# Kernel optimization log

Measured on AMD Instinct MI355X. Metric: run time of the kernel, lower is better.

Reference implementation:

```python
import jax, jax.numpy as jnp
import numpy as np

HIDDEN_DIM = 8


def setup_inputs() -> dict:
    key = jax.random.key(0)
    ks = jax.random.split(key, 10)
    B, S, C, H = 2048, 200, 25, HIDDEN_DIM
    s = 0.1
    return {
        "x": jax.random.normal(ks[0], (B, S, C), jnp.float32),
        "delay_W": jax.random.normal(ks[1], (S, C), jnp.float32) * s,
        "delay_b": jax.random.normal(ks[2], (S,), jnp.float32) * s,
        "U_W": jax.random.normal(ks[3], (H, C), jnp.float32) * s,
        "U_b": jax.random.normal(ks[4], (H,), jnp.float32) * s,
        "A_W": jax.random.normal(ks[5], (H, H), jnp.float32) * s,
        "B_W": jax.random.normal(ks[6], (H, C), jnp.float32) * s,
        "B_b": jax.random.normal(ks[7], (H,), jnp.float32) * s,
        "out_W": jax.random.normal(ks[8], (C, H), jnp.float32) * s,
        "out_b": jax.random.normal(ks[9], (C,), jnp.float32) * s,
    }


def reference(x, delay_W, delay_b, U_W, U_b, A_W, B_W, B_b, out_W, out_b):
    # x: [B, S, C] -> [S, B, C]
    xt = jnp.swapaxes(x, 0, 1)
    S, B, C = xt.shape
    # synaptic delay: each source timestep t distributes its signal over
    # all output timesteps via a softmax over the TIMESTEPS axis.
    logits = xt @ delay_W.T + delay_b                # [S, B, S]
    w = jax.nn.softmax(logits, axis=-1)              # [S, B, S_out]
    x_del = jnp.einsum('tbc,tbs->sbc', xt, w)        # [S_out, B, C]
    # SSM inputs
    u = x_del @ U_W.T + U_b                          # [S, B, H]
    b = jax.nn.sigmoid(x_del @ B_W.T + B_b)          # [S, B, H]

    # linear recurrence h_t = h_{t-1} A^T + b_t * u_t, h_0 = 0
    def step(h, bu):
        b_t, u_t = bu
        h = h @ A_W.T + b_t * u_t
        return h, h

    h0 = jnp.zeros((B, HIDDEN_DIM), xt.dtype)
    _, hs = jax.lax.scan(step, h0, (b, u))           # [S, B, H]
    out = hs @ out_W.T + out_b                       # [S, B, C]
    return jnp.swapaxes(out, 0, 1)                   # [B, S, C]
```

## Files before the change

kernel.cpp:

```cpp
#include <hip/hip_runtime.h>

#define NB 2048
#define S_ 200
#define C_ 25
#define H_ 8
#define WROWS 208
#define STR 28
#define NSTRIP 13
#define NSTILE 13
#define NPAIR 7
#define XDS 28
#define WFRAG (13 * 64 * 4)

typedef __bf16   bf16x8 __attribute__((ext_vector_type(8)));
typedef float    f32x4  __attribute__((ext_vector_type(4)));
typedef unsigned uint4v __attribute__((ext_vector_type(4)));

struct Frag { bf16x8 hi, lo; };

__device__ __forceinline__ unsigned short f2bf(float f) {
    unsigned u = __builtin_bit_cast(unsigned, f);
    return (unsigned short)((u + 0x7FFFu + ((u >> 16) & 1u)) >> 16);
}
__device__ __forceinline__ float bfh2f(unsigned short h) {
    return __builtin_bit_cast(float, (unsigned)h << 16);
}
__device__ __forceinline__ unsigned hi_pair(unsigned d0, unsigned d1) {
    return (d0 & 0xFFFFu) | (d1 << 16);
}
__device__ __forceinline__ unsigned lo_pair(unsigned d0, unsigned d1) {
    return (d0 >> 16) | (d1 & 0xFFFF0000u);
}
__device__ __forceinline__ Frag build_frag8(uint4v d0, uint4v d1) {
    uint4v h, l;
    h.x = hi_pair(d0.x, d0.y); h.y = hi_pair(d0.z, d0.w);
    h.z = hi_pair(d1.x, d1.y); h.w = hi_pair(d1.z, d1.w);
    l.x = lo_pair(d0.x, d0.y); l.y = lo_pair(d0.z, d0.w);
    l.z = lo_pair(d1.x, d1.y); l.w = lo_pair(d1.z, d1.w);
    Frag f;
    f.hi = __builtin_bit_cast(bf16x8, h);
    f.lo = __builtin_bit_cast(bf16x8, l);
    return f;
}
__device__ __forceinline__ bf16x8 build_hi8(uint4v d0, uint4v d1) {
    uint4v h;
    h.x = hi_pair(d0.x, d0.y); h.y = hi_pair(d0.z, d0.w);
    h.z = hi_pair(d1.x, d1.y); h.w = hi_pair(d1.z, d1.w);
    return __builtin_bit_cast(bf16x8, h);
}
__device__ __forceinline__ f32x4 mfma16(bf16x8 a, bf16x8 b, f32x4 c) {
    return __builtin_amdgcn_mfma_f32_16x16x32_bf16(a, b, c, 0, 0, 0);
}
__device__ __forceinline__ f32x4 mfma_split(const Frag& a, const Frag& b, f32x4 c) {
    c = mfma16(a.hi, b.hi, c);
    c = mfma16(a.hi, b.lo, c);
    c = mfma16(a.lo, b.hi, c);
    return c;
}
__device__ __forceinline__ float fexp2(float x) {
    float r; asm("v_exp_f32 %0, %1" : "=v"(r) : "v"(x)); return r;
}
__device__ __forceinline__ float flog2(float x) {
    float r; asm("v_log_f32 %0, %1" : "=v"(r) : "v"(x)); return r;
}
__device__ __forceinline__ unsigned cvt_pk_bf16(float vlo, float vhi) {
    unsigned r; asm("v_cvt_pk_bf16_f32 %0, %1, %2" : "=v"(r) : "v"(vlo), "v"(vhi)); return r;
}
__device__ __forceinline__ float lo16f(unsigned p) { return __builtin_bit_cast(float, p << 16); }
__device__ __forceinline__ float hi16f(unsigned p) { return __builtin_bit_cast(float, p & 0xFFFF0000u); }
__device__ __forceinline__ void pack_hl2(float v0, float v1, unsigned& d0, unsigned& d1) {
    unsigned hp = cvt_pk_bf16(v0, v1);
    float r0 = v0 - lo16f(hp);
    float r1 = v1 - hi16f(hp);
    unsigned lp = cvt_pk_bf16(r0, r1);
    d0 = (hp & 0xFFFFu) | (lp << 16);
    d1 = (hp >> 16) | (lp & 0xFFFF0000u);
}

__device__ __forceinline__ void xpose_quads(unsigned& a0, unsigned& a1,
                                            unsigned& b0, unsigned& b1) {
    asm("v_permlane32_swap_b32 %0, %1" : "+v"(a0), "+v"(b0));
    asm("v_permlane32_swap_b32 %0, %1" : "+v"(a1), "+v"(b1));
    asm("v_permlane16_swap_b32 %0, %1" : "+v"(a0), "+v"(b0));
    asm("v_permlane16_swap_b32 %0, %1" : "+v"(a1), "+v"(b1));
}

template<bool GUARD>
__device__ __forceinline__ void build_b2h(const unsigned* X32p, int pair, int q, int n,
                                          bf16x8 b2h[2]) {
#pragma unroll
    for (int ct = 0; ct < 2; ++ct) {
        const int c = ct * 16 + n;
        uint4v d0, d1;
#pragma unroll
        for (int j = 0; j < 4; ++j) {
            int t2 = pair * 32 + q * 8 + j;
            unsigned v;
            if (GUARD) v = (t2 < WROWS) ? X32p[t2 * STR + c] : 0u;
            else       v = X32p[t2 * STR + c];
            ((unsigned*)&d0)[j] = v;
        }
#pragma unroll
        for (int j = 0; j < 4; ++j) {
            int t2 = pair * 32 + q * 8 + 4 + j;
            unsigned v;
            if (GUARD) v = (t2 < WROWS) ? X32p[t2 * STR + c] : 0u;
            else       v = X32p[t2 * STR + c];
            ((unsigned*)&d1)[j] = v;
        }
        b2h[ct] = build_hi8(d0, d1);
    }
}

__global__ void prep_w_kernel(const float* __restrict__ delay_W,
                              const float* __restrict__ A_W,
                              unsigned* __restrict__ ws) {
    const float LOG2E = 1.44269504088896340736f;
    unsigned* Whi = ws;
    unsigned* Wlo = ws + WFRAG;
    for (int idx = blockIdx.x * 256 + threadIdx.x; idx < WFRAG; idx += gridDim.x * 256) {
        int d = idx & 3, lane = (idx >> 2) & 63, sv = idx >> 8;
        int q = lane >> 4, nn = lane & 15;
        int s  = sv * 16 + nn;
        int c0 = q * 8 + 2 * d;
        float v0 = (s < S_ && c0     < C_) ? delay_W[s * C_ + c0]     * LOG2E : 0.f;
        float v1 = (s < S_ && c0 + 1 < C_) ? delay_W[s * C_ + c0 + 1] * LOG2E : 0.f;
        unsigned short h0 = f2bf(v0), h1 = f2bf(v1);
        unsigned short l0 = f2bf(v0 - bfh2f(h0)), l1 = f2bf(v1 - bfh2f(h1));
        Whi[idx] = (unsigned)h0 | ((unsigned)h1 << 16);
        Wlo[idx] = (unsigned)l0 | ((unsigned)l1 << 16);
    }
    __shared__ float A2s[64];
    __shared__ float A4s[64];
    if (blockIdx.x == 0) {
        float* A2g = (float*)(ws + 2 * WFRAG);
        float* A4g = (float*)(ws + 2 * WFRAG + 64);
        float* A8g = (float*)(ws + 2 * WFRAG + 128);
        const int i = threadIdx.x >> 3, j = threadIdx.x & 7;
        if (threadIdx.x < 64) {
            float s = 0.f;
            for (int k = 0; k < 8; ++k) s = fmaf(A_W[i * 8 + k], A_W[k * 8 + j], s);
            A2s[threadIdx.x] = s; A2g[threadIdx.x] = s;
        }
        __syncthreads();
        if (threadIdx.x < 64) {
            float s = 0.f;
            for (int k = 0; k < 8; ++k) s = fmaf(A2s[i * 8 + k], A2s[k * 8 + j], s);
            A4s[threadIdx.x] = s; A4g[threadIdx.x] = s;
        }
        __syncthreads();
        if (threadIdx.x < 64) {
            float s = 0.f;
            for (int k = 0; k < 8; ++k) s = fmaf(A4s[i * 8 + k], A4s[k * 8 + j], s);
            A8g[threadIdx.x] = s;
        }
    }
}

__global__ __launch_bounds__(256, 5) void ssm_syn_delay_kernel(
    const float* __restrict__ x,       const unsigned* __restrict__ ws,
    const float* __restrict__ delay_b, const float* __restrict__ U_W,
    const float* __restrict__ U_b,     const float* __restrict__ A_W,
    const float* __restrict__ B_W,     const float* __restrict__ B_b,
    const float* __restrict__ out_W,   const float* __restrict__ out_b,
    float* __restrict__ out)
{
    __shared__ __align__(16) unsigned X32[WROWS * STR + 4];
    __shared__ __align__(16) float lsed[WROWS];
    __shared__ __align__(16) float dbs_l[WROWS];

    const int tid  = threadIdx.x;
    const int wid  = tid >> 6;
    const int lane = tid & 63;
    const int q    = lane >> 4;
    const int n    = lane & 15;
    const int b    = blockIdx.x;
    const float* xb = x + (size_t)b * (S_ * C_);
    const unsigned* Whi = ws;
    const unsigned* Wlo = ws + WFRAG;
    const float* A2g = (const float*)(ws + 2 * WFRAG);
    const float* A4g = (const float*)(ws + 2 * WFRAG + 64);
    const float* A8g = (const float*)(ws + 2 * WFRAG + 128);

    for (int i = tid; i < WROWS * 7; i += 256) {
        int r = i / 7, cg = i - r * 7;
        f32x4 v = {0.f, 0.f, 0.f, 0.f};
        if (r < S_) {
            if (cg < 6)       __builtin_memcpy(&v, &xb[r * C_ + cg * 4], 16);
            else              v[0] = xb[r * C_ + 24];
        }
        unsigned e0, e1, e2, e3;
        pack_hl2(v[0], v[1], e0, e1);
        pack_hl2(v[2], v[3], e2, e3);
        uint4v p = {e0, e1, e2, e3};
        *(uint4v*)&X32[r * STR + cg * 4] = p;
    }
    if (tid == 0) {
        uint4v z = {0u, 0u, 0u, 0u};
        *(uint4v*)&X32[WROWS * STR] = z;
    }
    for (int i = tid; i < WROWS; i += 256)
        dbs_l[i] = (i < S_) ? delay_b[i] * 1.44269504088896340736f : -1e30f;
    __syncthreads();

    for (int st = wid; st < NSTRIP; st += 4) {
        const int t = st * 16 + n;
        const uint4v* xp = (const uint4v*)&X32[t * STR + q * 8];
        Frag fa = build_frag8(xp[0], xp[1]);
        float rs0 = 0.f, rs1 = 0.f, rs2 = 0.f, rs3 = 0.f;
        for (int sv = 0; sv < NSTILE; ++sv) {
            Frag fb;
            fb.hi = __builtin_bit_cast(bf16x8, *(const uint4v*)&Whi[(sv * 64 + lane) * 4]);
            fb.lo = __builtin_bit_cast(bf16x8, *(const uint4v*)&Wlo[(sv * 64 + lane) * 4]);
            f32x4 L = {0.f, 0.f, 0.f, 0.f};
            L = mfma_split(fa, fb, L);
            const float dbv = dbs_l[sv * 16 + n];
            rs0 += fexp2(L[0] + dbv);
            rs1 += fexp2(L[1] + dbv);
            rs2 += fexp2(L[2] + dbv);
            rs3 += fexp2(L[3] + dbv);
        }
#pragma unroll
        for (int off = 1; off < 16; off <<= 1) {
            rs0 += __shfl_xor(rs0, off);
            rs1 += __shfl_xor(rs1, off);
            rs2 += __shfl_xor(rs2, off);
            rs3 += __shfl_xor(rs3, off);
        }
        if (n < 4) {
            float v = (n == 0) ? rs0 : (n == 1) ? rs1 : (n == 2) ? rs2 : rs3;
            lsed[st * 16 + q * 4 + n] = flog2(v);
        }
    }
    __syncthreads();

    f32x4 acc[4][2];
#pragma unroll
    for (int i = 0; i < 4; ++i)
#pragma unroll
        for (int j = 0; j < 2; ++j) acc[i][j] = f32x4{0.f, 0.f, 0.f, 0.f};

    for (int pair = 0; pair < NPAIR; ++pair) {
        const int sA = 2 * pair, sB = sA + 1;
        const bool bval = (sB < NSTRIP);
        const uint4v* xpA = (const uint4v*)&X32[(sA * 16 + n) * STR + q * 8];
        Frag faA = build_frag8(xpA[0], xpA[1]);
        Frag faB;
        if (bval) {
            const uint4v* xpB = (const uint4v*)&X32[(sB * 16 + n) * STR + q * 8];
            faB = build_frag8(xpB[0], xpB[1]);
        }
        f32x4 lseA = *(const f32x4*)&lsed[sA * 16 + q * 4];
        f32x4 lseB = bval ? *(const f32x4*)&lsed[sB * 16 + q * 4] : f32x4{0,0,0,0};
        bf16x8 b2h[2];
        if (pair < 6) build_b2h<false>(X32, pair, q, n, b2h);
        else          build_b2h<true >(X32, pair, q, n, b2h);

#pragma unroll
        for (int si = 0; si < 4; ++si) {
            const int sv = wid + 4 * si;
            if (sv >= NSTILE) continue;
            Frag fb;
            fb.hi = __builtin_bit_cast(bf16x8, *(const uint4v*)&Whi[(sv * 64 + lane) * 4]);
            fb.lo = __builtin_bit_cast(bf16x8, *(const uint4v*)&Wlo[(sv * 64 + lane) * 4]);
            const float dbv = dbs_l[sv * 16 + n];
            unsigned pA0, pA1, qA0, qA1;
            {
                f32x4 L = {0.f, 0.f, 0.f, 0.f};
                L = mfma_split(faA, fb, L);
                float e0 = fexp2(L[0] + dbv - lseA[0]);
                float e1 = fexp2(L[1] + dbv - lseA[1]);
                float e2 = fexp2(L[2] + dbv - lseA[2]);
                float e3 = fexp2(L[3] + dbv - lseA[3]);
                pA0 = cvt_pk_bf16(e0, e1);
                pA1 = cvt_pk_bf16(e2, e3);
                qA0 = cvt_pk_bf16(e0 - lo16f(pA0), e1 - hi16f(pA0));
                qA1 = cvt_pk_bf16(e2 - lo16f(pA1), e3 - hi16f(pA1));
            }
            unsigned pB0 = 0u, pB1 = 0u, qB0 = 0u, qB1 = 0u;
            if (bval) {
                f32x4 L = {0.f, 0.f, 0.f, 0.f};
                L = mfma_split(faB, fb, L);
                float e0 = fexp2(L[0] + dbv - lseB[0]);
                float e1 = fexp2(L[1] + dbv - lseB[1]);
                float e2 = fexp2(L[2] + dbv - lseB[2]);
                float e3 = fexp2(L[3] + dbv - lseB[3]);
                pB0 = cvt_pk_bf16(e0, e1);
                pB1 = cvt_pk_bf16(e2, e3);
                qB0 = cvt_pk_bf16(e0 - lo16f(pB0), e1 - hi16f(pB0));
                qB1 = cvt_pk_bf16(e2 - lo16f(pB1), e3 - hi16f(pB1));
            }
            xpose_quads(pA0, pA1, pB0, pB1);
            xpose_quads(qA0, qA1, qB0, qB1);
            uint4v hv = {pA0, pA1, pB0, pB1};
            uint4v lv = {qA0, qA1, qB0, qB1};
            bf16x8 a2h = __builtin_bit_cast(bf16x8, hv);
            bf16x8 a2l = __builtin_bit_cast(bf16x8, lv);
#pragma unroll
            for (int ct = 0; ct < 2; ++ct) {
                f32x4 c4 = acc[si][ct];
                c4 = mfma16(a2h, b2h[ct], c4);
                c4 = mfma16(a2l, b2h[ct], c4);
                acc[si][ct] = c4;
            }
        }
    }
    __syncthreads();

    float* fbse = (float*)&X32[0];
    float* xdelf = fbse;
    float* pbuf  = fbse;
    float* r1    = fbse + 1600;
    float* r2    = fbse + 3200;
#pragma unroll
    for (int si = 0; si < 4; ++si) {
        const int sv = wid + 4 * si;
        if (sv >= NSTILE) continue;
#pragma unroll
        for (int ct = 0; ct < 2; ++ct) {
            const int c = ct * 16 + n;
            if (c < C_) {
#pragma unroll
                for (int r = 0; r < 4; ++r) {
                    const int s = sv * 16 + q * 4 + r;
                    if (s < S_) xdelf[s * XDS + c] = acc[si][ct][r];
                }
            }
        }
    }
    __syncthreads();

    {
        float a[24], a24 = 0.f;
        const bool act = tid < S_;
        if (act) {
            const f32x4* ar = (const f32x4*)&xdelf[tid * XDS];
#pragma unroll
            for (int k = 0; k < 6; ++k) *(f32x4*)&a[k * 4] = ar[k];
            a24 = xdelf[tid * XDS + 24];
        }
        __syncthreads();
        if (act) {
            const int s = tid;
#pragma unroll
            for (int h = 0; h < H_; ++h) {
                float uu = fmaf(a24, U_W[h * C_ + 24], U_b[h]);
                float bb = fmaf(a24, B_W[h * C_ + 24], B_b[h]);
#pragma unroll
                for (int i = 0; i < 24; ++i) {
                    uu = fmaf(a[i], U_W[h * C_ + i], uu);
                    bb = fmaf(a[i], B_W[h * C_ + i], bb);
                }
                float sg_ = 1.0f / (1.0f + __expf(-bb));
                pbuf[s * H_ + h] = uu * sg_;
            }
        }
    }
    __syncthreads();

    for (int i2 = tid; i2 < S_ * H_; i2 += 256) {
        const int s = i2 >> 3, i = i2 & 7;
        float v = pbuf[i2];
        if (s > 0) {
            const float* pm = &pbuf[(s - 1) * H_];
#pragma unroll
            for (int j = 0; j < H_; ++j) v = fmaf(A_W[i * H_ + j], pm[j], v);
        }
        r1[i2] = v;
    }
    __syncthreads();
    for (int i2 = tid; i2 < S_ * H_; i2 += 256) {
        const int s = i2 >> 3, i = i2 & 7;
        float v = r1[i2];
        if (s > 1) {
            const float* pm = &r1[(s - 2) * H_];
#pragma unroll
            for (int j = 0; j < H_; ++j) v = fmaf(A2g[i * H_ + j], pm[j], v);
        }
        r2[i2] = v;
    }
    __syncthreads();
    for (int i2 = tid; i2 < S_ * H_; i2 += 256) {
        const int s = i2 >> 3, i = i2 & 7;
        float v = r2[i2];
        if (s > 3) {
            const float* pm = &r2[(s - 4) * H_];
#pragma unroll
            for (int j = 0; j < H_; ++j) v = fmaf(A4g[i * H_ + j], pm[j], v);
        }
        pbuf[i2] = v;
    }
    __syncthreads();
    if (tid < 64) {
        const int r = tid >> 3, i = tid & 7;
        float A8r[H_];
#pragma unroll
        for (int j = 0; j < H_; ++j) A8r[j] = A8g[i * H_ + j];
        float h = 0.f;
        for (int k = 0; k < 25; ++k) {
            const int s = 8 * k + r;
            float v = pbuf[s * H_ + i];
#pragma unroll
            for (int j = 0; j < H_; ++j) v = fmaf(A8r[j], __shfl(h, j, 8), v);
            h = v;
            r1[s * H_ + i] = h;
        }
    }
    __syncthreads();

    float* ob_ptr = out + (size_t)b * (S_ * C_);
    for (int i = tid; i < S_ * C_; i += 256) {
        int s = i / C_, c = i - s * C_;
        const f32x4* pr = (const f32x4*)&r1[s * H_];
        const f32x4* wr = (const f32x4*)&out_W[c * H_];
        f32x4 h0 = pr[0], h1 = pr[1];
        f32x4 w0 = wr[0], w1 = wr[1];
        float v = out_b[c];
        v = fmaf(h0[0], w0[0], v);
        v = fmaf(h0[1], w0[1], v);
        v = fmaf(h0[2], w0[2], v);
        v = fmaf(h0[3], w0[3], v);
        v = fmaf(h1[0], w1[0], v);
        v = fmaf(h1[1], w1[1], v);
        v = fmaf(h1[2], w1[2], v);
        v = fmaf(h1[3], w1[3], v);
        ob_ptr[i] = v;
    }
}

extern "C" void kernel_launch(void* const* d_in, const int* in_sizes, int n_in,
                              void* d_out, int out_size, void* d_ws, size_t ws_size,
                              hipStream_t stream) {
    const float* x       = (const float*)d_in[0];
    const float* delay_W = (const float*)d_in[1];
    const float* delay_b = (const float*)d_in[2];
    const float* U_W     = (const float*)d_in[3];
    const float* U_b     = (const float*)d_in[4];
    const float* A_W     = (const float*)d_in[5];
    const float* B_W     = (const float*)d_in[6];
    const float* B_b     = (const float*)d_in[7];
    const float* out_W   = (const float*)d_in[8];
    const float* out_b   = (const float*)d_in[9];
    float* out = (float*)d_out;
    unsigned* ws = (unsigned*)d_ws;

    prep_w_kernel<<<4, 256, 0, stream>>>(delay_W, A_W, ws);
    ssm_syn_delay_kernel<<<NB, 256, 0, stream>>>(
        x, ws, delay_b, U_W, U_b, A_W, B_W, B_b, out_W, out_b, out);
}
```

Measured before the change: 231.1 us.

## Precompute transposed x B-fragments in LDS and batch logsumexp strips per W tile

Builds the transposed bf16 x fragments for the second GEMM once per block into a new shared-memory table, so each pair iteration reads one vector per tile instead of doing eight scalar strided loads and packing. The logsumexp pass now keeps up to four strip fragments in registers and loops over W tiles once, so each W fragment is loaded once per wave rather than once per strip. Occupancy hint drops from 5 to 4 waves per SIMD to make room for the added registers and about 14 KB of extra LDS.

```diff
diff --git a/kernel.cpp b/kernel.cpp
--- a/kernel.cpp
+++ b/kernel.cpp
@@ -11,6 +11,7 @@
 #define NPAIR 7
 #define XDS 28
 #define WFRAG (13 * 64 * 4)
+#define B2N (NPAIR * 2 * 64 * 4)
 
 typedef __bf16   bf16x8 __attribute__((ext_vector_type(8)));
 typedef float    f32x4  __attribute__((ext_vector_type(4)));
@@ -42,12 +43,6 @@
     f.lo = __builtin_bit_cast(bf16x8, l);
     return f;
 }
-__device__ __forceinline__ bf16x8 build_hi8(uint4v d0, uint4v d1) {
-    uint4v h;
-    h.x = hi_pair(d0.x, d0.y); h.y = hi_pair(d0.z, d0.w);
-    h.z = hi_pair(d1.x, d1.y); h.w = hi_pair(d1.z, d1.w);
-    return __builtin_bit_cast(bf16x8, h);
-}
 __device__ __forceinline__ f32x4 mfma16(bf16x8 a, bf16x8 b, f32x4 c) {
     return __builtin_amdgcn_mfma_f32_16x16x32_bf16(a, b, c, 0, 0, 0);
 }
@@ -83,33 +78,6 @@
     asm("v_permlane32_swap_b32 %0, %1" : "+v"(a1), "+v"(b1));
     asm("v_permlane16_swap_b32 %0, %1" : "+v"(a0), "+v"(b0));
     asm("v_permlane16_swap_b32 %0, %1" : "+v"(a1), "+v"(b1));
-}
-
-template<bool GUARD>
-__device__ __forceinline__ void build_b2h(const unsigned* X32p, int pair, int q, int n,
-                                          bf16x8 b2h[2]) {
-#pragma unroll
-    for (int ct = 0; ct < 2; ++ct) {
-        const int c = ct * 16 + n;
-        uint4v d0, d1;
-#pragma unroll
-        for (int j = 0; j < 4; ++j) {
-            int t2 = pair * 32 + q * 8 + j;
-            unsigned v;
-            if (GUARD) v = (t2 < WROWS) ? X32p[t2 * STR + c] : 0u;
-            else       v = X32p[t2 * STR + c];
-            ((unsigned*)&d0)[j] = v;
-        }
-#pragma unroll
-        for (int j = 0; j < 4; ++j) {
-            int t2 = pair * 32 + q * 8 + 4 + j;
-            unsigned v;
-            if (GUARD) v = (t2 < WROWS) ? X32p[t2 * STR + c] : 0u;
-            else       v = X32p[t2 * STR + c];
-            ((unsigned*)&d1)[j] = v;
-        }
-        b2h[ct] = build_hi8(d0, d1);
-    }
 }
 
 __global__ void prep_w_kernel(const float* __restrict__ delay_W,
@@ -157,7 +125,7 @@
     }
 }
 
-__global__ __launch_bounds__(256, 5) void ssm_syn_delay_kernel(
+__global__ __launch_bounds__(256, 4) void ssm_syn_delay_kernel(
     const float* __restrict__ x,       const unsigned* __restrict__ ws,
     const float* __restrict__ delay_b, const float* __restrict__ U_W,
     const float* __restrict__ U_b,     const float* __restrict__ A_W,
@@ -166,6 +134,7 @@
     float* __restrict__ out)
 {
     __shared__ __align__(16) unsigned X32[WROWS * STR + 4];
+    __shared__ __align__(16) unsigned B2T[B2N];
     __shared__ __align__(16) float lsed[WROWS];
     __shared__ __align__(16) float dbs_l[WROWS];
 
@@ -203,33 +172,62 @@
         dbs_l[i] = (i < S_) ? delay_b[i] * 1.44269504088896340736f : -1e30f;
     __syncthreads();
 
-    for (int st = wid; st < NSTRIP; st += 4) {
-        const int t = st * 16 + n;
-        const uint4v* xp = (const uint4v*)&X32[t * STR + q * 8];
-        Frag fa = build_frag8(xp[0], xp[1]);
-        float rs0 = 0.f, rs1 = 0.f, rs2 = 0.f, rs3 = 0.f;
+    for (int idx = tid; idx < B2N; idx += 256) {
+        const int k  = idx & 3;
+        const int ln = (idx >> 2) & 63;
+        const int ct = (idx >> 8) & 1;
+        const int pr = idx >> 9;
+        const int t0 = pr * 32 + (ln >> 4) * 8 + 2 * k;
+        const int c  = ct * 16 + (ln & 15);
+        unsigned u0 = (t0     < WROWS) ? X32[t0 * STR + c] : 0u;
+        unsigned u1 = (t0 + 1 < WROWS) ? X32[(t0 + 1) * STR + c] : 0u;
+        B2T[idx] = hi_pair(u0, u1);
+    }
+
+    {
+        Frag fa[4];
+        f32x4 rs[4];
+#pragma unroll
+        for (int k2 = 0; k2 < 4; ++k2) {
+            rs[k2] = f32x4{0.f, 0.f, 0.f, 0.f};
+            const int st = wid + 4 * k2;
+            if (st < NSTRIP) {
+                const uint4v* xp = (const uint4v*)&X32[(st * 16 + n) * STR + q * 8];
+                fa[k2] = build_frag8(xp[0], xp[1]);
+            }
+        }
         for (int sv = 0; sv < NSTILE; ++sv) {
             Frag fb;
             fb.hi = __builtin_bit_cast(bf16x8, *(const uint4v*)&Whi[(sv * 64 + lane) * 4]);
             fb.lo = __builtin_bit_cast(bf16x8, *(const uint4v*)&Wlo[(sv * 64 + lane) * 4]);
-            f32x4 L = {0.f, 0.f, 0.f, 0.f};
-            L = mfma_split(fa, fb, L);
             const float dbv = dbs_l[sv * 16 + n];
-            rs0 += fexp2(L[0] + dbv);
-            rs1 += fexp2(L[1] + dbv);
-            rs2 += fexp2(L[2] + dbv);
-            rs3 += fexp2(L[3] + dbv);
-        }
-#pragma unroll
-        for (int off = 1; off < 16; off <<= 1) {
-            rs0 += __shfl_xor(rs0, off);
-            rs1 += __shfl_xor(rs1, off);
-            rs2 += __shfl_xor(rs2, off);
-            rs3 += __shfl_xor(rs3, off);
-        }
-        if (n < 4) {
-            float v = (n == 0) ? rs0 : (n == 1) ? rs1 : (n == 2) ? rs2 : rs3;
-            lsed[st * 16 + q * 4 + n] = flog2(v);
+#pragma unroll
+            for (int k2 = 0; k2 < 4; ++k2) {
+                if (wid + 4 * k2 >= NSTRIP) continue;
+                f32x4 L = {0.f, 0.f, 0.f, 0.f};
+                L = mfma_split(fa[k2], fb, L);
+                rs[k2][0] += fexp2(L[0] + dbv);
+                rs[k2][1] += fexp2(L[1] + dbv);
+                rs[k2][2] += fexp2(L[2] + dbv);
+                rs[k2][3] += fexp2(L[3] + dbv);
+            }
+        }
+#pragma unroll
+        for (int k2 = 0; k2 < 4; ++k2) {
+            const int st = wid + 4 * k2;
+            if (st >= NSTRIP) continue;
+            float r0 = rs[k2][0], r1 = rs[k2][1], r2 = rs[k2][2], r3 = rs[k2][3];
+#pragma unroll
+            for (int off = 1; off < 16; off <<= 1) {
+                r0 += __shfl_xor(r0, off);
+                r1 += __shfl_xor(r1, off);
+                r2 += __shfl_xor(r2, off);
+                r3 += __shfl_xor(r3, off);
+            }
+            if (n < 4) {
+                float v = (n == 0) ? r0 : (n == 1) ? r1 : (n == 2) ? r2 : r3;
+                lsed[st * 16 + q * 4 + n] = flog2(v);
+            }
         }
     }
     __syncthreads();
@@ -253,8 +251,10 @@
         f32x4 lseA = *(const f32x4*)&lsed[sA * 16 + q * 4];
         f32x4 lseB = bval ? *(const f32x4*)&lsed[sB * 16 + q * 4] : f32x4{0,0,0,0};
         bf16x8 b2h[2];
-        if (pair < 6) build_b2h<false>(X32, pair, q, n, b2h);
-        else          build_b2h<true >(X32, pair, q, n, b2h);
+#pragma unroll
+        for (int ct = 0; ct < 2; ++ct)
+            b2h[ct] = __builtin_bit_cast(bf16x8,
+                        *(const uint4v*)&B2T[((pair * 2 + ct) * 64 + lane) * 4]);
 
 #pragma unroll
         for (int si = 0; si < 4; ++si) {
```

After: 228.5 us. Within noise of the previous version (-1.1%).
